# Kernel tuning notes

Hardware: AMD Instinct MI355X
Metric: run time of the kernel (lower is better)

The kernel has to match this reference:

```python
import jax, jax.numpy as jnp
import numpy as np

DIM = 1024
HEADS = 16
HEAD_DIM = DIM // HEADS
MAX_REL = 1024
B, N = 4, 1024


def setup_inputs() -> dict:
    key = jax.random.key(0)
    k1, k2, k3, k4, k5 = jax.random.split(key, 5)
    x = jax.random.normal(k1, (B, N, DIM), dtype=jnp.float32)
    W_qkv = jax.random.normal(k2, (3 * DIM, DIM), dtype=jnp.float32) * 0.02
    W_proj = jax.random.normal(k3, (DIM, DIM), dtype=jnp.float32) * 0.02
    b_proj = jnp.zeros((DIM,), dtype=jnp.float32)
    Er = jax.random.normal(k4, (MAX_REL, HEAD_DIM), dtype=jnp.float32)
    return {"x": x, "W_qkv": W_qkv, "W_proj": W_proj, "b_proj": b_proj, "Er": Er}


def _relative_skew(S_rel):
    # S_rel: [B, H, L, L] -> pad a zero column on the left, reshape, drop first row
    Bb, H, L, _ = S_rel.shape
    S = jnp.pad(S_rel, ((0, 0), (0, 0), (0, 0), (1, 0)))  # [B,H,L,L+1]
    S = S.reshape(Bb, H, L + 1, L)
    return S[:, :, 1:, :]


def reference(x, W_qkv, W_proj, b_proj, Er):
    Bb, Nn, C = x.shape
    scale = HEAD_DIM ** (-0.5)
    qkv = jnp.einsum('bnc,fc->bnf', x, W_qkv)           # [B,N,3C]
    qkv = qkv.reshape(Bb, Nn, 3, HEADS, HEAD_DIM)
    q = jnp.transpose(qkv[:, :, 0], (0, 2, 1, 3))        # [B,H,N,d]
    k = jnp.transpose(qkv[:, :, 1], (0, 2, 1, 3))
    v = jnp.transpose(qkv[:, :, 2], (0, 2, 1, 3))
    content = jnp.einsum('bhnd,bhmd->bhnm', q, k)        # [B,H,N,N]
    er_seq = Er[:Nn]                                     # [N,d]
    rel = jnp.einsum('bhnd,md->bhnm', q, er_seq)         # [B,H,N,N]
    rel = _relative_skew(rel)
    score = (content + rel) * scale
    causal = jnp.triu(jnp.ones((Nn, Nn), dtype=bool), k=1)
    score = jnp.where(causal, -jnp.inf, score)
    probs = jax.nn.softmax(score, axis=-1)
    out = jnp.einsum('bhnm,bhmd->bhnd', probs, v)        # [B,H,N,d]
    out = jnp.transpose(out, (0, 2, 1, 3)).reshape(Bb, Nn, C)
    return jnp.einsum('bnc,oc->bno', out, W_proj) + b_proj
```

## Files before the change

### kernel.cpp

```cpp
#include <hip/hip_runtime.h>
#include <math.h>

#define BATCH 4
#define SEQ   1024
#define DIM_C 1024
#define HEADS 16
#define HDIM  64
#define F3    3072

typedef short bf8 __attribute__((ext_vector_type(8)));
typedef float f32x4 __attribute__((ext_vector_type(4)));

__device__ __forceinline__ ushort f2bf(float f) {
    union { float f; unsigned u; } c; c.f = f;
    unsigned u = c.u + 0x7fffu + ((c.u >> 16) & 1u);
    return (ushort)(u >> 16);
}
__device__ __forceinline__ float bf2f(ushort s) {
    union { unsigned u; float f; } c; c.u = ((unsigned)s) << 16;
    return c.f;
}

__device__ __forceinline__ void stage16(const ushort* g, ushort* l) {
    __builtin_amdgcn_global_load_lds(
        (const __attribute__((address_space(1))) unsigned int*)g,
        (__attribute__((address_space(3))) unsigned int*)l, 16, 0, 0);
}

__global__ __launch_bounds__(256) void cvt_all_kernel(
    const float* __restrict__ x, const float* __restrict__ wqkv,
    const float* __restrict__ wproj, const float* __restrict__ er,
    ushort* __restrict__ xb, ushort* __restrict__ wqkvb,
    ushort* __restrict__ wprojb, ushort* __restrict__ erb)
{
    const int blk = blockIdx.x;
    const float* src; ushort* dst; size_t off;
    if (blk < 2048)      { src = x;     dst = xb;     off = (size_t)blk * 2048; }
    else if (blk < 3584) { src = wqkv;  dst = wqkvb;  off = (size_t)(blk - 2048) * 2048; }
    else if (blk < 4096) { src = wproj; dst = wprojb; off = (size_t)(blk - 3584) * 2048; }
    else                 { src = er;    dst = erb;    off = (size_t)(blk - 4096) * 2048; }
    size_t i = off + (size_t)threadIdx.x * 8;
    float4 v0 = *(const float4*)&src[i];
    float4 v1 = *(const float4*)&src[i + 4];
    ushort o[8];
    o[0] = f2bf(v0.x); o[1] = f2bf(v0.y); o[2] = f2bf(v0.z); o[3] = f2bf(v0.w);
    o[4] = f2bf(v1.x); o[5] = f2bf(v1.y); o[6] = f2bf(v1.z); o[7] = f2bf(v1.w);
    *(uint4*)&dst[i] = *(uint4*)o;
}

__device__ __forceinline__ void gemm_core(
    const ushort* __restrict__ a, const ushort* __restrict__ b,
    ushort* As, ushort* Bs, int m0, int f0, int t, f32x4 (&acc)[4][4])
{
    const int lane = t & 63, w = t >> 6;
    const int lc = lane & 15, g4 = lane >> 4;
    const int wm = (w >> 1) * 64, wn = (w & 1) * 64;
    const int rowS = w * 32 + (lane >> 2);
    const int kkS  = (lane & 3) * 8;

    for (int kt = 0; kt < 32; ++kt) {
        const int k0 = kt * 32;
        __syncthreads();
        #pragma unroll
        for (int ii = 0; ii < 2; ++ii) {
            stage16(&a[(size_t)(m0 + rowS + ii * 16) * 1024 + k0 + kkS],
                    &As[(w * 2 + ii) * 512]);
            stage16(&b[(size_t)(f0 + rowS + ii * 16) * 1024 + k0 + kkS],
                    &Bs[(w * 2 + ii) * 512]);
        }
        __syncthreads();
        bf8 af[4], bfr[4];
        #pragma unroll
        for (int mb = 0; mb < 4; ++mb)
            af[mb] = *(const bf8*)&As[(wm + mb * 16 + lc) * 32 + g4 * 8];
        #pragma unroll
        for (int nb = 0; nb < 4; ++nb)
            bfr[nb] = *(const bf8*)&Bs[(wn + nb * 16 + lc) * 32 + g4 * 8];
        #pragma unroll
        for (int mb = 0; mb < 4; ++mb)
            #pragma unroll
            for (int nb = 0; nb < 4; ++nb)
                acc[mb][nb] = __builtin_amdgcn_mfma_f32_16x16x32_bf16(
                    af[mb], bfr[nb], acc[mb][nb], 0, 0, 0);
    }
}

__global__ __launch_bounds__(256) void gemm_qkv_mfma(
    const ushort* __restrict__ xb, const ushort* __restrict__ wb,
    ushort* __restrict__ qp, ushort* __restrict__ kp, ushort* __restrict__ vp)
{
    __shared__ __align__(16) ushort As[128 * 32];
    __shared__ __align__(16) ushort Bs[128 * 32];
    const int t = threadIdx.x;
    const int m0 = blockIdx.y * 128, f0 = blockIdx.x * 128;
    f32x4 acc[4][4];
    #pragma unroll
    for (int mb = 0; mb < 4; ++mb)
        #pragma unroll
        for (int nb = 0; nb < 4; ++nb) acc[mb][nb] = (f32x4){0.f, 0.f, 0.f, 0.f};

    gemm_core(xb, wb, As, Bs, m0, f0, t, acc);

    const int lane = t & 63, w = t >> 6;
    const int lc = lane & 15, g4 = lane >> 4;
    const int wm = (w >> 1) * 64, wn = (w & 1) * 64;
    const int s = f0 >> 10;
    #pragma unroll
    for (int mb = 0; mb < 4; ++mb)
        #pragma unroll
        for (int nb = 0; nb < 4; ++nb) {
            const int f = f0 + wn + nb * 16 + lc;
            const int h = (f >> 6) & 15, d = f & 63;
            if (s == 2) {
                const int m = m0 + wm + mb * 16 + g4 * 4;
                const int b = m >> 10, n = m & 1023;
                ushort4 o;
                o.x = f2bf(acc[mb][nb][0]); o.y = f2bf(acc[mb][nb][1]);
                o.z = f2bf(acc[mb][nb][2]); o.w = f2bf(acc[mb][nb][3]);
                *(ushort4*)&vp[(((size_t)(b * 16 + h)) * 64 + d) * 1024 + n] = o;
            } else {
                ushort* dst = (s == 0) ? qp : kp;
                #pragma unroll
                for (int i = 0; i < 4; ++i) {
                    const int m = m0 + wm + mb * 16 + g4 * 4 + i;
                    const int b = m >> 10, n = m & 1023;
                    dst[(((size_t)(b * 16 + h)) * 1024 + n) * 64 + d] = f2bf(acc[mb][nb][i]);
                }
            }
        }
}

__global__ __launch_bounds__(256) void gemm_proj_mfma(
    const ushort* __restrict__ ab, const ushort* __restrict__ wb,
    const float* __restrict__ bias, float* __restrict__ y)
{
    __shared__ __align__(16) ushort As[128 * 32];
    __shared__ __align__(16) ushort Bs[128 * 32];
    const int t = threadIdx.x;
    const int m0 = blockIdx.y * 128, f0 = blockIdx.x * 128;
    f32x4 acc[4][4];
    #pragma unroll
    for (int mb = 0; mb < 4; ++mb)
        #pragma unroll
        for (int nb = 0; nb < 4; ++nb) acc[mb][nb] = (f32x4){0.f, 0.f, 0.f, 0.f};

    gemm_core(ab, wb, As, Bs, m0, f0, t, acc);

    const int lane = t & 63, w = t >> 6;
    const int lc = lane & 15, g4 = lane >> 4;
    const int wm = (w >> 1) * 64, wn = (w & 1) * 64;
    #pragma unroll
    for (int mb = 0; mb < 4; ++mb)
        #pragma unroll
        for (int nb = 0; nb < 4; ++nb) {
            const int f = f0 + wn + nb * 16 + lc;
            const float bv = bias[f];
            #pragma unroll
            for (int i = 0; i < 4; ++i) {
                const int m = m0 + wm + mb * 16 + g4 * 4 + i;
                y[(size_t)m * 1024 + f] = acc[mb][nb][i] + bv;
            }
        }
}

__global__ __launch_bounds__(512, 4) void attn_mfma_kernel(
    const ushort* __restrict__ qg, const ushort* __restrict__ kg,
    const ushort* __restrict__ vtg, const ushort* __restrict__ erg,
    ushort* __restrict__ pOd, float* __restrict__ pL)
{
    __shared__ __align__(16) ushort k_s[2][64][64];
    __shared__ __align__(16) ushort vt_s[2][64][64];
    __shared__ __align__(16) ushort e_s[4][64][64];
    __shared__ __align__(16) ushort p_s[8][16][64];

    const int t = threadIdx.x;
    const int w = t >> 6, lane = t & 63;
    const int lc = lane & 15, g4 = lane >> 4;
    const int b = blockIdx.z, h = blockIdx.y;
    const int u = blockIdx.x;
    const int cum[9] = {0, 1, 2, 4, 6, 9, 12, 16, 20};
    int bx = 0;
    #pragma unroll
    for (int j = 1; j < 8; ++j) if (u >= cum[j]) bx = j;
    const int part = u - cum[bx];
    const int t0 = part * 4;
    const int t1 = min(t0 + 4, 2 * bx + 2);

    const int n0 = bx * 128;
    const int n0w = n0 + w * 16;
    const int ch0 = 14 + t0 - 2 * bx;

    const ushort* qb  = qg  + ((size_t)(b * 16 + h)) * 65536;
    const ushort* kb  = kg  + ((size_t)(b * 16 + h)) * 65536;
    const ushort* vtb = vtg + ((size_t)(b * 16 + h)) * 65536;

    const int srow = lane >> 3;
    const int scol = ((lane & 7) ^ srow) * 8;
    const int sr0  = w * 8 + srow;
    const int rsw  = (lc & 7) * 8;

    stage16(&kb[(size_t)(t0 * 64 + sr0) * 64 + scol], &k_s[0][w * 8][0]);
    stage16(&vtb[(size_t)sr0 * 1024 + t0 * 64 + scol], &vt_s[0][w * 8][0]);
    #pragma unroll
    for (int cc = 0; cc < 3; ++cc) {
        const int ch = ch0 + cc;
        int gr = ch * 64 + sr0;
        gr = (gr > 1023) ? 1023 : gr;
        stage16(&erg[(size_t)gr * 64 + scol], &e_s[ch & 3][w * 8][0]);
    }

    bf8 qf[2];
    #pragma unroll
    for (int c = 0; c < 2; ++c)
        qf[c] = *(const bf8*)&qb[(size_t)(n0w + lc) * 64 + c * 32 + g4 * 8];

    asm volatile("s_waitcnt vmcnt(0)" ::: "memory");
    __builtin_amdgcn_s_barrier();

    const f32x4 z4 = {0.f, 0.f, 0.f, 0.f};
    f32x4 od[4] = {z4, z4, z4, z4};
    float lrow[4] = {0.f, 0.f, 0.f, 0.f};
    int cur = 0;

    for (int tt = t0; tt < t1; ++tt) {
        const int m0 = tt * 64;

        if (tt + 1 < t1) {
            const int m1 = m0 + 64;
            const int nxt = cur ^ 1;
            stage16(&kb[(size_t)(m1 + sr0) * 64 + scol], &k_s[nxt][w * 8][0]);
            stage16(&vtb[(size_t)sr0 * 1024 + m1 + scol], &vt_s[nxt][w * 8][0]);
            const int chN = 17 + tt - 2 * bx;
            int gr = chN * 64 + sr0;
            gr = (gr > 1023) ? 1023 : gr;
            stage16(&erg[(size_t)gr * 64 + scol], &e_s[chN & 3][w * 8][0]);
            asm volatile("s_waitcnt vmcnt(3)" ::: "memory");
        } else {
            asm volatile("s_waitcnt vmcnt(0)" ::: "memory");
        }
        __builtin_amdgcn_s_barrier();

        f32x4 sc[4] = {z4, z4, z4, z4};
        #pragma unroll
        for (int jt = 0; jt < 4; ++jt)
            #pragma unroll
            for (int c = 0; c < 2; ++c) {
                bf8 kf = *(const bf8*)&k_s[cur][jt * 16 + lc][((c * 4 + g4) * 8) ^ rsw];
                sc[jt] = __builtin_amdgcn_mfma_f32_16x16x32_bf16(qf[c], kf, sc[jt], 0, 0, 0);
            }

        const int eBw = 1008 + m0 - n0 - 16 * w;
        f32x4 rc[5] = {z4, z4, z4, z4, z4};
        #pragma unroll
        for (int jr = 0; jr < 5; ++jr) {
            const int g  = eBw + jr * 16 + lc;
            const int s3 = (g >> 6) & 3;
            const int r  = g & 63;
            #pragma unroll
            for (int c = 0; c < 2; ++c) {
                bf8 ef = *(const bf8*)&e_s[s3][r][((c * 4 + g4) * 8) ^ rsw];
                rc[jr] = __builtin_amdgcn_mfma_f32_16x16x32_bf16(qf[c], ef, rc[jr], 0, 0, 0);
            }
        }

        #pragma unroll
        for (int i = 0; i < 4; ++i) {
            const int row = g4 * 4 + i;
            const int n = n0w + row;
            const int src = (lc + 15 - row) & 15;
            float sh[5];
            #pragma unroll
            for (int jr = 0; jr < 5; ++jr)
                sh[jr] = __shfl(rc[jr][i], src, 16);
            #pragma unroll
            for (int jt = 0; jt < 4; ++jt) {
                const float rel = (lc > row) ? sh[jt + 1] : sh[jt];
                const float s = (sc[jt][i] + rel) * 0.125f;
                const int m = m0 + jt * 16 + lc;
                const float p = (m <= n) ? __expf(s) : 0.f;
                const int blk = (jt * 2 + (lc >> 3)) ^ (row & 7);
                p_s[w][row][blk * 8 + (lc & 7)] = f2bf(p);
                lrow[i] += p;
            }
        }
        asm volatile("s_waitcnt lgkmcnt(0)" ::: "memory");

        bf8 pf[2];
        #pragma unroll
        for (int c = 0; c < 2; ++c)
            pf[c] = *(const bf8*)&p_s[w][lc][((c * 4 + g4) ^ (lc & 7)) * 8];
        #pragma unroll
        for (int dt = 0; dt < 4; ++dt)
            #pragma unroll
            for (int c = 0; c < 2; ++c) {
                bf8 vf = *(const bf8*)&vt_s[cur][dt * 16 + lc][((c * 4 + g4) * 8) ^ rsw];
                od[dt] = __builtin_amdgcn_mfma_f32_16x16x32_bf16(pf[c], vf, od[dt], 0, 0, 0);
            }

        __builtin_amdgcn_s_barrier();
        cur ^= 1;
    }

    #pragma unroll
    for (int off = 1; off < 16; off <<= 1)
        #pragma unroll
        for (int i = 0; i < 4; ++i)
            lrow[i] += __shfl_xor(lrow[i], off, 16);

    const size_t pbase = (size_t)((b * 16 + h) * 20 + u);
    #pragma unroll
    for (int i = 0; i < 4; ++i) {
        const int nl = w * 16 + g4 * 4 + i;
        #pragma unroll
        for (int dt = 0; dt < 4; ++dt)
            pOd[pbase * 8192 + nl * 64 + dt * 16 + lc] = f2bf(od[dt][i]);
        if (lc == 0) pL[pbase * 128 + nl] = lrow[i];
    }
}

__global__ __launch_bounds__(256) void attn_combine_kernel(
    const ushort* __restrict__ pOd, const float* __restrict__ pL,
    ushort* __restrict__ attnb)
{
    const int tid = blockIdx.x * 256 + threadIdx.x;
    const int d8 = tid & 7;
    const int n  = (tid >> 3) & 1023;
    const int bh = tid >> 13;
    const int bx = n >> 7, nl = n & 127;
    const int cum[9] = {0, 1, 2, 4, 6, 9, 12, 16, 20};
    const int u0 = cum[bx], pc = cum[bx + 1] - cum[bx];

    float acc[8] = {0.f, 0.f, 0.f, 0.f, 0.f, 0.f, 0.f, 0.f};
    float lsum = 0.f;
    for (int j = 0; j < pc; ++j) {
        const size_t base = (size_t)(bh * 20 + u0 + j);
        uint4 pv = *(const uint4*)&pOd[base * 8192 + nl * 64 + d8 * 8];
        const ushort* pp = (const ushort*)&pv;
        #pragma unroll
        for (int e = 0; e < 8; ++e) acc[e] += bf2f(pp[e]);
        lsum += pL[base * 128 + nl];
    }
    const float inv = 1.f / lsum;
    ushort o[8];
    #pragma unroll
    for (int e = 0; e < 8; ++e) o[e] = f2bf(acc[e] * inv);
    const int b = bh >> 4, h = bh & 15;
    *(uint4*)&attnb[((size_t)(b * 1024) + n) * 1024 + h * 64 + d8 * 8] = *(uint4*)o;
}

extern "C" void kernel_launch(void* const* d_in, const int* in_sizes, int n_in,
                              void* d_out, int out_size, void* d_ws, size_t ws_size,
                              hipStream_t stream)
{
    const float* x     = (const float*)d_in[0];
    const float* Wqkv  = (const float*)d_in[1];
    const float* Wproj = (const float*)d_in[2];
    const float* bproj = (const float*)d_in[3];
    const float* Er    = (const float*)d_in[4];
    float* out = (float*)d_out;

    const size_t per = (size_t)BATCH * HEADS * SEQ * HDIM;
    ushort* xb     = (ushort*)d_ws;
    ushort* wqkvb  = xb + (size_t)4194304;
    ushort* wprojb = wqkvb + (size_t)3145728;
    ushort* erb    = wprojb + (size_t)1048576;
    ushort* qw     = erb + (size_t)65536;
    ushort* kw     = qw + per;
    ushort* vw     = kw + per;
    ushort* attnb  = vw + per;
    ushort* pOd    = attnb + per;
    float*  pL     = (float*)(pOd + (size_t)64 * 20 * 8192);

    cvt_all_kernel<<<dim3(4128), 256, 0, stream>>>(
        x, Wqkv, Wproj, Er, xb, wqkvb, wprojb, erb);

    gemm_qkv_mfma<<<dim3(F3 / 128, (BATCH * SEQ) / 128), 256, 0, stream>>>(
        xb, wqkvb, qw, kw, vw);

    attn_mfma_kernel<<<dim3(20, HEADS, BATCH), 512, 0, stream>>>(
        qw, kw, vw, erb, pOd, pL);

    attn_combine_kernel<<<dim3(2048), 256, 0, stream>>>(pOd, pL, attnb);

    gemm_proj_mfma<<<dim3(DIM_C / 128, (BATCH * SEQ) / 128), 256, 0, stream>>>(
        attnb, wprojb, bproj, out);
}
```

Baseline: 186.9 us.

## Swizzle GEMM LDS layout and compute V projection transposed for coalesced stores

The shared-memory tiles in the GEMM core get an XOR swizzle on the 8-element column chunk, applied consistently to the global-to-LDS staging and to the MFMA fragment reads, to cut LDS bank conflicts. The QKV kernel now computes V blocks as W·xᵀ by swapping the A/B operands, so each lane's accumulator column maps to contiguous sequence positions in the transposed V layout. Q/K blocks keep the original mapping. The grid mapping relies on bx>=16 meaning V, which assumes a particular launch shape and is fragile if the launch changes.

```diff
diff --git a/kernel.cpp b/kernel.cpp
--- a/kernel.cpp
+++ b/kernel.cpp
@@ -56,7 +56,8 @@
     const int lc = lane & 15, g4 = lane >> 4;
     const int wm = (w >> 1) * 64, wn = (w & 1) * 64;
     const int rowS = w * 32 + (lane >> 2);
-    const int kkS  = (lane & 3) * 8;
+    const int kkS  = ((lane & 3) ^ ((rowS >> 1) & 3)) * 8;
+    const int coff = (g4 ^ ((lc >> 1) & 3)) * 8;
 
     for (int kt = 0; kt < 32; ++kt) {
         const int k0 = kt * 32;
@@ -72,10 +73,10 @@
         bf8 af[4], bfr[4];
         #pragma unroll
         for (int mb = 0; mb < 4; ++mb)
-            af[mb] = *(const bf8*)&As[(wm + mb * 16 + lc) * 32 + g4 * 8];
+            af[mb] = *(const bf8*)&As[(wm + mb * 16 + lc) * 32 + coff];
         #pragma unroll
         for (int nb = 0; nb < 4; ++nb)
-            bfr[nb] = *(const bf8*)&Bs[(wn + nb * 16 + lc) * 32 + g4 * 8];
+            bfr[nb] = *(const bf8*)&Bs[(wn + nb * 16 + lc) * 32 + coff];
         #pragma unroll
         for (int mb = 0; mb < 4; ++mb)
             #pragma unroll
@@ -92,34 +93,47 @@
     __shared__ __align__(16) ushort As[128 * 32];
     __shared__ __align__(16) ushort Bs[128 * 32];
     const int t = threadIdx.x;
-    const int m0 = blockIdx.y * 128, f0 = blockIdx.x * 128;
+    const int bx = blockIdx.x, by = blockIdx.y;
+    const bool isV = (bx >= 16);
+    const int m0 = isV ? 2048 + (bx - 16) * 128 : by * 128;
+    const int f0 = isV ? by * 128 : bx * 128;
+    const ushort* A = isV ? wb : xb;
+    const ushort* B = isV ? xb : wb;
+
     f32x4 acc[4][4];
     #pragma unroll
     for (int mb = 0; mb < 4; ++mb)
         #pragma unroll
         for (int nb = 0; nb < 4; ++nb) acc[mb][nb] = (f32x4){0.f, 0.f, 0.f, 0.f};
 
-    gemm_core(xb, wb, As, Bs, m0, f0, t, acc);
+    gemm_core(A, B, As, Bs, m0, f0, t, acc);
 
     const int lane = t & 63, w = t >> 6;
     const int lc = lane & 15, g4 = lane >> 4;
     const int wm = (w >> 1) * 64, wn = (w & 1) * 64;
-    const int s = f0 >> 10;
-    #pragma unroll
-    for (int mb = 0; mb < 4; ++mb)
-        #pragma unroll
-        for (int nb = 0; nb < 4; ++nb) {
-            const int f = f0 + wn + nb * 16 + lc;
-            const int h = (f >> 6) & 15, d = f & 63;
-            if (s == 2) {
-                const int m = m0 + wm + mb * 16 + g4 * 4;
-                const int b = m >> 10, n = m & 1023;
-                ushort4 o;
-                o.x = f2bf(acc[mb][nb][0]); o.y = f2bf(acc[mb][nb][1]);
-                o.z = f2bf(acc[mb][nb][2]); o.w = f2bf(acc[mb][nb][3]);
-                *(ushort4*)&vp[(((size_t)(b * 16 + h)) * 64 + d) * 1024 + n] = o;
-            } else {
-                ushort* dst = (s == 0) ? qp : kp;
+    if (isV) {
+        #pragma unroll
+        for (int mb = 0; mb < 4; ++mb)
+            #pragma unroll
+            for (int nb = 0; nb < 4; ++nb) {
+                const int ncol = f0 + wn + nb * 16 + lc;
+                const int bi = ncol >> 10, nl = ncol & 1023;
+                #pragma unroll
+                for (int i = 0; i < 4; ++i) {
+                    const int vrow = m0 + wm + mb * 16 + g4 * 4 + i - 2048;
+                    const int h = vrow >> 6, d = vrow & 63;
+                    vp[(((size_t)(bi * 16 + h)) * 64 + d) * 1024 + nl] = f2bf(acc[mb][nb][i]);
+                }
+            }
+    } else {
+        const int s = f0 >> 10;
+        ushort* dst = (s == 0) ? qp : kp;
+        #pragma unroll
+        for (int mb = 0; mb < 4; ++mb)
+            #pragma unroll
+            for (int nb = 0; nb < 4; ++nb) {
+                const int f = f0 + wn + nb * 16 + lc;
+                const int h = (f >> 6) & 15, d = f & 63;
                 #pragma unroll
                 for (int i = 0; i < 4; ++i) {
                     const int m = m0 + wm + mb * 16 + g4 * 4 + i;
@@ -127,7 +141,7 @@
                     dst[(((size_t)(b * 16 + h)) * 1024 + n) * 64 + d] = f2bf(acc[mb][nb][i]);
                 }
             }
-        }
+    }
 }
 
 __global__ __launch_bounds__(256) void gemm_proj_mfma(
```

Result: slower. 194.0 us (median of 2 runs) (+3.8%).
